# Optimization experiments

Hardware: AMD Instinct MI355X
Metric: run time of the kernel (lower is better)

## Reference

```python
import jax, jax.numpy as jnp
import numpy as np


def _pairwise_dist(x, y):
    # x: [B, N, D], y: [B, M, D] -> [B, N, M] Euclidean distances.
    # Use ||x||^2 + ||y||^2 - 2<x,y> (gram form) to avoid the [B,N,M,D]
    # broadcast intermediate the torch code materializes.
    x2 = jnp.sum(x * x, axis=-1)  # [B, N]
    y2 = jnp.sum(y * y, axis=-1)  # [B, M]
    xy = jnp.einsum('bnd,bmd->bnm', x, y)  # [B, N, M]
    sq = x2[:, :, None] + y2[:, None, :] - 2.0 * xy
    return jnp.sqrt(jnp.maximum(sq, 1e-12))


def setup_inputs() -> dict:
    key = jax.random.key(0)
    k1, k2 = jax.random.split(key)
    B, N, M, D = 8, 4096, 4096, 64
    pred = jax.random.normal(k1, (B, N, D), dtype=jnp.float32)
    label = jax.random.normal(k2, (B, M, D), dtype=jnp.float32)
    return {"pred": pred, "label": label}


def reference(pred, label):
    dis = _pairwise_dist(pred, label)  # [B, N, M]
    dis_xy = jnp.max(jnp.min(dis, axis=2))  # max over all (b, n) of min over m
    dis_yx = jnp.max(jnp.min(dis, axis=1))  # max over all (b, m) of min over n
    return dis_xy + dis_yx
```

## Files before the change

kernel.cpp:

```cpp
#include <hip/hip_runtime.h>
#include <hip/hip_bf16.h>

#define B_ 8
#define N_ 4096
#define M_ 4096
#define D_ 64
#define BNT (B_ * N_)
#define BMT (B_ * M_)
#define TA 64
#define TB 128
#define NT 512
#define CHUNK_TILES 8
#define CHUNK_B (TB * CHUNK_TILES)
#define MCHUNK (M_ / CHUNK_B)
#define NBLK (N_ / TA * MCHUNK * B_)

typedef short bf16x8 __attribute__((ext_vector_type(8)));
typedef float f32x4 __attribute__((ext_vector_type(4)));

__device__ __forceinline__ unsigned short f2bf(float f) {
  __hip_bfloat16 h = __float2bfloat16(f);
  return *reinterpret_cast<unsigned short*>(&h);
}

__device__ __forceinline__ unsigned fkey(float f) {
  unsigned b = __float_as_uint(f);
  return b ^ ((unsigned)((int)b >> 31) | 0x80000000u);
}
__device__ __forceinline__ float funkey(unsigned k) {
  unsigned b = (k & 0x80000000u) ? (k ^ 0x80000000u) : ~k;
  return __uint_as_float(b);
}

__device__ __forceinline__ bf16x8 cvt8(float4 lo, float4 hi) {
  union { unsigned short u[8]; bf16x8 v; } r;
  r.u[0] = f2bf(lo.x); r.u[1] = f2bf(lo.y); r.u[2] = f2bf(lo.z); r.u[3] = f2bf(lo.w);
  r.u[4] = f2bf(hi.x); r.u[5] = f2bf(hi.y); r.u[6] = f2bf(hi.z); r.u[7] = f2bf(hi.w);
  return r.v;
}

__device__ __forceinline__ void gload_lds16(const void* g, void* l) {
  __builtin_amdgcn_global_load_lds(
      (const __attribute__((address_space(1))) unsigned int*)g,
      (__attribute__((address_space(3))) unsigned int*)l, 16, 0, 0);
}

template <int ROWS, bool BF>
__device__ __forceinline__ void stage_tile(const void* gsrc, unsigned short* lds,
                                           int t, int srcpat) {
  if (BF) {
    constexpr int PER_WAVE = (ROWS * 128 / 1024) / (NT / 64);
    const char* gp = (const char*)gsrc;
    int w = t >> 6;
#pragma unroll
    for (int i = 0; i < PER_WAVE; i++) {
      int q = w * PER_WAVE + i;
      gload_lds16(gp + q * 1024 + srcpat, (char*)lds + q * 1024);
    }
  } else {
    const float4* g4 = (const float4*)gsrc;
#pragma unroll
    for (int i = 0; i < ROWS * 16 / NT; i++) {
      int off = i * NT + t;
      float4 v = g4[off];
      int row = off >> 4;
      int cb = (off & 15) * 8;
      int ba = (row * 128 + cb) ^ ((row & 7) << 4);
      ushort4 p;
      p.x = f2bf(v.x); p.y = f2bf(v.y); p.z = f2bf(v.z); p.w = f2bf(v.w);
      *(ushort4*)((char*)lds + ba) = p;
    }
  }
}

template <bool CONV>
__global__ __launch_bounds__(256) void prep_kernel(
    const float* __restrict__ pred, const float* __restrict__ label,
    unsigned short* __restrict__ predbf, unsigned short* __restrict__ labelbf,
    float* __restrict__ x2, float* __restrict__ y2,
    unsigned* __restrict__ minN, unsigned* __restrict__ minM,
    unsigned* __restrict__ gmax) {
  int t = threadIdx.x;
  int lane = t & 15;
  long row = (long)blockIdx.x * 16 + (t >> 4);
  bool isA = row < BNT;
  const float4* src;
  unsigned short* bdst;
  float* ndst;
  unsigned* mdst;
  if (isA) {
    src = (const float4*)(pred + row * D_);
    bdst = predbf + row * D_;
    ndst = x2 + row;
    mdst = minN + row;
  } else {
    long r2 = row - BNT;
    src = (const float4*)(label + r2 * D_);
    bdst = labelbf + r2 * D_;
    ndst = y2 + r2;
    mdst = minM + r2;
  }
  float4 v = src[lane];
  if (CONV) {
    float s = isA ? -2.f : 1.f;
    ushort4 p;
    p.x = f2bf(s * v.x); p.y = f2bf(s * v.y);
    p.z = f2bf(s * v.z); p.w = f2bf(s * v.w);
    *(ushort4*)(bdst + lane * 4) = p;
  }
  float s = v.x * v.x + v.y * v.y + v.z * v.z + v.w * v.w;
  s += __shfl_xor(s, 1);
  s += __shfl_xor(s, 2);
  s += __shfl_xor(s, 4);
  s += __shfl_xor(s, 8);
  if (lane == 0) {
    *ndst = s;
    *mdst = 0xFFFFFFFFu;
  }
  if (blockIdx.x == 0 && t < 2) gmax[t] = 0u;
}

template <bool BF>
__global__ __launch_bounds__(NT) void fused_kernel(
    const void* __restrict__ Asrc, const void* __restrict__ Bsrc,
    const float* __restrict__ x2g, const float* __restrict__ y2g,
    unsigned* __restrict__ minN, unsigned* __restrict__ minM) {
  __shared__ alignas(16) unsigned short Bs[2][TB * 64];
  __shared__ float y2l[CHUNK_B];
  __shared__ float cmSlab[CHUNK_B];
  __shared__ float red[8][TA];

  const int t = threadIdx.x;
  const int bid = blockIdx.x;
  const int k = bid & 7;
  const int j = bid >> 3;
  const int b = k;
  const int yq = j >> 6;
  const int x = j & 63;
  const int a0 = x * TA;
  const int m0 = yq * CHUNK_B;

  const int w = t >> 6, l = t & 63;
  const int g = l >> 4, c = l & 15;
  const int srcpat = (l >> 3) * 128 + (((l & 7) * 16) ^ ((l >> 3) << 4));

  const size_t rowbytes = BF ? 128 : 256;
  const char* Bgl = (const char*)Bsrc + ((size_t)b * M_ + m0) * rowbytes;

  ((float2*)y2l)[t] = ((const float2*)(y2g + (size_t)b * M_ + m0))[t];

  stage_tile<TB, BF>(Bgl, Bs[0], t, srcpat);

  bf16x8 af[2][4];
  if (BF) {
    const unsigned short* Ab =
        (const unsigned short*)Asrc + ((size_t)b * N_ + a0) * D_;
#pragma unroll
    for (int kk = 0; kk < 2; kk++)
#pragma unroll
      for (int mi = 0; mi < 4; mi++)
        af[kk][mi] =
            *(const bf16x8*)(Ab + (size_t)(mi * 16 + c) * D_ + kk * 32 + g * 8);
  } else {
    const float* Af = (const float*)Asrc + ((size_t)b * N_ + a0) * D_;
#pragma unroll
    for (int kk = 0; kk < 2; kk++)
#pragma unroll
      for (int mi = 0; mi < 4; mi++) {
        const float4* p =
            (const float4*)(Af + (size_t)(mi * 16 + c) * D_ + kk * 32 + g * 8);
        float4 lo = p[0], hi = p[1];
        lo.x *= -2.f; lo.y *= -2.f; lo.z *= -2.f; lo.w *= -2.f;
        hi.x *= -2.f; hi.y *= -2.f; hi.z *= -2.f; hi.w *= -2.f;
        af[kk][mi] = cvt8(lo, hi);
      }
  }

  float x2v[4][4];
#pragma unroll
  for (int mi = 0; mi < 4; mi++)
#pragma unroll
    for (int e = 0; e < 4; e++)
      x2v[mi][e] = x2g[(size_t)b * N_ + a0 + mi * 16 + g * 4 + e];

  float rmin[4][4];
#pragma unroll
  for (int mi = 0; mi < 4; mi++)
#pragma unroll
    for (int e = 0; e < 4; e++) rmin[mi][e] = INFINITY;

  __syncthreads();

  for (int it = 0; it < CHUNK_TILES; it++) {
    if (it + 1 < CHUNK_TILES)
      stage_tile<TB, BF>(Bgl + (size_t)(it + 1) * TB * rowbytes,
                         Bs[(it + 1) & 1], t, srcpat);
    const char* Bcur = (const char*)(&Bs[it & 1][0]);

    const int r = w * 16 + c;
    const float nv = y2l[it * TB + r];
    bf16x8 b0 = *(const bf16x8*)(Bcur + ((r * 128 + g * 16) ^ ((r & 7) << 4)));
    bf16x8 b1 = *(const bf16x8*)(Bcur + ((r * 128 + 64 + g * 16) ^ ((r & 7) << 4)));

    f32x4 acc[4];
#pragma unroll
    for (int mi = 0; mi < 4; mi++) acc[mi] = (f32x4){nv, nv, nv, nv};
#pragma unroll
    for (int mi = 0; mi < 4; mi++)
      acc[mi] = __builtin_amdgcn_mfma_f32_16x16x32_bf16(af[0][mi], b0, acc[mi], 0, 0, 0);
#pragma unroll
    for (int mi = 0; mi < 4; mi++)
      acc[mi] = __builtin_amdgcn_mfma_f32_16x16x32_bf16(af[1][mi], b1, acc[mi], 0, 0, 0);

    float cs[4];
#pragma unroll
    for (int mi = 0; mi < 4; mi++) {
      float c0 = acc[mi][0] + x2v[mi][0];
      float c1 = acc[mi][1] + x2v[mi][1];
      float c2 = acc[mi][2] + x2v[mi][2];
      float c3 = acc[mi][3] + x2v[mi][3];
      cs[mi] = fminf(fminf(c0, c1), fminf(c2, c3));
#pragma unroll
      for (int e = 0; e < 4; e++)
        rmin[mi][e] = fminf(rmin[mi][e], acc[mi][e]);
    }
    float cm = fminf(fminf(cs[0], cs[1]), fminf(cs[2], cs[3]));
    cm = fminf(cm, __shfl_xor(cm, 16));
    cm = fminf(cm, __shfl_xor(cm, 32));
    if (g == 0) cmSlab[it * TB + r] = cm - nv;

    __syncthreads();
  }

#pragma unroll
  for (int mi = 0; mi < 4; mi++)
#pragma unroll
    for (int e = 0; e < 4; e++) {
      float r = rmin[mi][e];
      r = fminf(r, __shfl_xor(r, 1));
      r = fminf(r, __shfl_xor(r, 2));
      r = fminf(r, __shfl_xor(r, 4));
      r = fminf(r, __shfl_xor(r, 8));
      rmin[mi][e] = r;
    }
  if (c == 0) {
#pragma unroll
    for (int mi = 0; mi < 4; mi++)
#pragma unroll
      for (int e = 0; e < 4; e++)
        red[w][mi * 16 + g * 4 + e] = rmin[mi][e];
  }
  __syncthreads();
  if (t < TA) {
    float m = red[0][t];
#pragma unroll
    for (int i = 1; i < 8; i++) m = fminf(m, red[i][t]);
    atomicMin(&minN[(size_t)b * N_ + a0 + t], fkey(m));
  }
#pragma unroll
  for (int i = 0; i < CHUNK_B / NT; i++) {
    int r = i * NT + t;
    atomicMin(&minM[(size_t)b * M_ + m0 + r], fkey(cmSlab[r]));
  }
}

__global__ __launch_bounds__(256) void final1_kernel(
    const unsigned* __restrict__ minN, const unsigned* __restrict__ minM,
    const float* __restrict__ x2, const float* __restrict__ y2,
    unsigned* __restrict__ gmax) {
  int dir = blockIdx.x >> 5;
  int blk = blockIdx.x & 31;
  const unsigned* src = dir ? minM : minN;
  const float* nrm = dir ? y2 : x2;
  size_t base = (size_t)blk * 256;
  float mx = -INFINITY;
  {
    int i = threadIdx.x;
    uint4 k = ((const uint4*)src)[base + i];
    float4 nv = ((const float4*)nrm)[base + i];
    mx = fmaxf(mx, nv.x + funkey(k.x));
    mx = fmaxf(mx, nv.y + funkey(k.y));
    mx = fmaxf(mx, nv.z + funkey(k.z));
    mx = fmaxf(mx, nv.w + funkey(k.w));
  }
#pragma unroll
  for (int mask = 1; mask < 64; mask <<= 1) mx = fmaxf(mx, __shfl_xor(mx, mask));
  __shared__ float sm[4];
  if ((threadIdx.x & 63) == 0) sm[threadIdx.x >> 6] = mx;
  __syncthreads();
  if (threadIdx.x == 0) {
    mx = fmaxf(fmaxf(sm[0], sm[1]), fmaxf(sm[2], sm[3]));
    atomicMax(&gmax[dir], fkey(mx));
  }
}

__global__ void final2_kernel(const unsigned* __restrict__ gmax, float* __restrict__ out) {
  if (threadIdx.x == 0)
    out[0] = sqrtf(fmaxf(funkey(gmax[0]), 1e-12f)) +
             sqrtf(fmaxf(funkey(gmax[1]), 1e-12f));
}

extern "C" void kernel_launch(void* const* d_in, const int* in_sizes, int n_in,
                              void* d_out, int out_size, void* d_ws, size_t ws_size,
                              hipStream_t stream) {
  const float* pred = (const float*)d_in[0];
  const float* label = (const float*)d_in[1];
  char* ws = (char*)d_ws;

  const size_t bfBytes = (size_t)BNT * D_ * 2;
  const size_t needFast = 2 * bfBytes + (size_t)(BNT + BMT) * 8 + 64;

  if (ws_size >= needFast) {
    unsigned short* predbf = (unsigned short*)ws;
    unsigned short* labelbf = (unsigned short*)(ws + bfBytes);
    float* x2 = (float*)(ws + 2 * bfBytes);
    float* y2 = x2 + BNT;
    unsigned* minN = (unsigned*)(y2 + BMT);
    unsigned* minM = minN + BNT;
    unsigned* gmax = minM + BMT;

    prep_kernel<true><<<(BNT + BMT) / 16, 256, 0, stream>>>(
        pred, label, predbf, labelbf, x2, y2, minN, minM, gmax);
    fused_kernel<true><<<NBLK, NT, 0, stream>>>(
        predbf, labelbf, x2, y2, minN, minM);
    final1_kernel<<<64, 256, 0, stream>>>(minN, minM, x2, y2, gmax);
    final2_kernel<<<1, 64, 0, stream>>>(gmax, (float*)d_out);
  } else {
    float* x2 = (float*)ws;
    float* y2 = x2 + BNT;
    unsigned* minN = (unsigned*)(y2 + BMT);
    unsigned* minM = minN + BNT;
    unsigned* gmax = minM + BMT;

    prep_kernel<false><<<(BNT + BMT) / 16, 256, 0, stream>>>(
        pred, label, nullptr, nullptr, x2, y2, minN, minM, gmax);
    fused_kernel<false><<<NBLK, NT, 0, stream>>>(
        pred, label, x2, y2, minN, minM);
    final1_kernel<<<64, 256, 0, stream>>>(minN, minM, x2, y2, gmax);
    final2_kernel<<<1, 64, 0, stream>>>(gmax, (float*)d_out);
  }
}
```

Baseline: 72.70 us.

## Halve block size and stage B tiles via registers with two-deep prefetch

Drops the block to 256 threads, so each wave now covers two 16-row slices of every B tile, which doubles the MFMA work per wave. Global-to-LDS direct loads are replaced by register staging: tiles are prefetched two iterations ahead into registers, then written swizzled into LDS behind a lighter barrier. The aim is to hide global latency and cut barrier overhead per unit of work. In exchange it uses more registers, which may lower occupancy, and adds extra LDS write instructions.

```diff
diff --git a/kernel.cpp b/kernel.cpp
--- a/kernel.cpp
+++ b/kernel.cpp
@@ -9,7 +9,7 @@
 #define BMT (B_ * M_)
 #define TA 64
 #define TB 128
-#define NT 512
+#define NT 256
 #define CHUNK_TILES 8
 #define CHUNK_B (TB * CHUNK_TILES)
 #define MCHUNK (M_ / CHUNK_B)
@@ -39,37 +39,33 @@
   return r.v;
 }
 
-__device__ __forceinline__ void gload_lds16(const void* g, void* l) {
-  __builtin_amdgcn_global_load_lds(
-      (const __attribute__((address_space(1))) unsigned int*)g,
-      (__attribute__((address_space(3))) unsigned int*)l, 16, 0, 0);
-}
-
-template <int ROWS, bool BF>
-__device__ __forceinline__ void stage_tile(const void* gsrc, unsigned short* lds,
-                                           int t, int srcpat) {
-  if (BF) {
-    constexpr int PER_WAVE = (ROWS * 128 / 1024) / (NT / 64);
-    const char* gp = (const char*)gsrc;
-    int w = t >> 6;
-#pragma unroll
-    for (int i = 0; i < PER_WAVE; i++) {
-      int q = w * PER_WAVE + i;
-      gload_lds16(gp + q * 1024 + srcpat, (char*)lds + q * 1024);
+__device__ __forceinline__ void block_sync_lds() {
+  asm volatile("s_waitcnt lgkmcnt(0)" ::: "memory");
+  __builtin_amdgcn_s_barrier();
+  __builtin_amdgcn_sched_barrier(0);
+}
+
+template <bool BF>
+__device__ __forceinline__ void stage_load(const char* gtile, bf16x8* arr, int t) {
+#pragma unroll
+  for (int i = 0; i < 4; i++) {
+    int q = i * NT + t;
+    if (BF) {
+      arr[i] = *(const bf16x8*)(gtile + (size_t)q * 16);
+    } else {
+      const float4* p = (const float4*)(gtile + (size_t)q * 32);
+      arr[i] = cvt8(p[0], p[1]);
     }
-  } else {
-    const float4* g4 = (const float4*)gsrc;
-#pragma unroll
-    for (int i = 0; i < ROWS * 16 / NT; i++) {
-      int off = i * NT + t;
-      float4 v = g4[off];
-      int row = off >> 4;
-      int cb = (off & 15) * 8;
-      int ba = (row * 128 + cb) ^ ((row & 7) << 4);
-      ushort4 p;
-      p.x = f2bf(v.x); p.y = f2bf(v.y); p.z = f2bf(v.z); p.w = f2bf(v.w);
-      *(ushort4*)((char*)lds + ba) = p;
-    }
+  }
+}
+
+__device__ __forceinline__ void stage_write(unsigned short* lds, const bf16x8* arr, int t) {
+#pragma unroll
+  for (int i = 0; i < 4; i++) {
+    int q = i * NT + t;
+    int row = q >> 3, col = q & 7;
+    int dst = (row * 128 + col * 16) ^ ((row & 7) << 4);
+    *(bf16x8*)((char*)lds + dst) = arr[i];
   }
 }
 
@@ -128,28 +124,26 @@
   __shared__ alignas(16) unsigned short Bs[2][TB * 64];
   __shared__ float y2l[CHUNK_B];
   __shared__ float cmSlab[CHUNK_B];
-  __shared__ float red[8][TA];
+  __shared__ float red[4][TA];
 
   const int t = threadIdx.x;
   const int bid = blockIdx.x;
-  const int k = bid & 7;
+  const int b = bid & 7;
   const int j = bid >> 3;
-  const int b = k;
-  const int yq = j >> 6;
-  const int x = j & 63;
-  const int a0 = x * TA;
-  const int m0 = yq * CHUNK_B;
+  const int a0 = (j & 63) * TA;
+  const int m0 = (j >> 6) * CHUNK_B;
 
   const int w = t >> 6, l = t & 63;
   const int g = l >> 4, c = l & 15;
-  const int srcpat = (l >> 3) * 128 + (((l & 7) * 16) ^ ((l >> 3) << 4));
-
-  const size_t rowbytes = BF ? 128 : 256;
-  const char* Bgl = (const char*)Bsrc + ((size_t)b * M_ + m0) * rowbytes;
-
-  ((float2*)y2l)[t] = ((const float2*)(y2g + (size_t)b * M_ + m0))[t];
-
-  stage_tile<TB, BF>(Bgl, Bs[0], t, srcpat);
+
+  const size_t tilebytes = (size_t)TB * 64 * (BF ? 2 : 4);
+  const char* Bgl = (const char*)Bsrc + ((size_t)b * M_ + m0) * (BF ? 128 : 256);
+
+  ((float4*)y2l)[t] = ((const float4*)(y2g + (size_t)b * M_ + m0))[t];
+
+  bf16x8 stg[2][4];
+  stage_load<BF>(Bgl, stg[0], t);
+  stage_load<BF>(Bgl + tilebytes, stg[1], t);
 
   bf16x8 af[2][4];
   if (BF) {
@@ -189,47 +183,54 @@
 #pragma unroll
     for (int e = 0; e < 4; e++) rmin[mi][e] = INFINITY;
 
-  __syncthreads();
-
-  for (int it = 0; it < CHUNK_TILES; it++) {
-    if (it + 1 < CHUNK_TILES)
-      stage_tile<TB, BF>(Bgl + (size_t)(it + 1) * TB * rowbytes,
-                         Bs[(it + 1) & 1], t, srcpat);
+  stage_write(Bs[0], stg[0], t);
+  block_sync_lds();
+
+#pragma unroll
+  for (int it = 0; it < CHUNK_TILES; ++it) {
+    if (it + 2 < CHUNK_TILES)
+      stage_load<BF>(Bgl + (size_t)(it + 2) * tilebytes, stg[it & 1], t);
+
     const char* Bcur = (const char*)(&Bs[it & 1][0]);
-
-    const int r = w * 16 + c;
-    const float nv = y2l[it * TB + r];
-    bf16x8 b0 = *(const bf16x8*)(Bcur + ((r * 128 + g * 16) ^ ((r & 7) << 4)));
-    bf16x8 b1 = *(const bf16x8*)(Bcur + ((r * 128 + 64 + g * 16) ^ ((r & 7) << 4)));
-
-    f32x4 acc[4];
-#pragma unroll
-    for (int mi = 0; mi < 4; mi++) acc[mi] = (f32x4){nv, nv, nv, nv};
-#pragma unroll
-    for (int mi = 0; mi < 4; mi++)
-      acc[mi] = __builtin_amdgcn_mfma_f32_16x16x32_bf16(af[0][mi], b0, acc[mi], 0, 0, 0);
-#pragma unroll
-    for (int mi = 0; mi < 4; mi++)
-      acc[mi] = __builtin_amdgcn_mfma_f32_16x16x32_bf16(af[1][mi], b1, acc[mi], 0, 0, 0);
-
-    float cs[4];
-#pragma unroll
-    for (int mi = 0; mi < 4; mi++) {
-      float c0 = acc[mi][0] + x2v[mi][0];
-      float c1 = acc[mi][1] + x2v[mi][1];
-      float c2 = acc[mi][2] + x2v[mi][2];
-      float c3 = acc[mi][3] + x2v[mi][3];
-      cs[mi] = fminf(fminf(c0, c1), fminf(c2, c3));
-#pragma unroll
-      for (int e = 0; e < 4; e++)
-        rmin[mi][e] = fminf(rmin[mi][e], acc[mi][e]);
+#pragma unroll
+    for (int h = 0; h < 2; ++h) {
+      const int r = w * 32 + h * 16 + c;
+      const float nv = y2l[it * TB + r];
+      bf16x8 b0 = *(const bf16x8*)(Bcur + ((r * 128 + g * 16) ^ ((r & 7) << 4)));
+      bf16x8 b1 = *(const bf16x8*)(Bcur + ((r * 128 + 64 + g * 16) ^ ((r & 7) << 4)));
+
+      f32x4 acc[4];
+#pragma unroll
+      for (int mi = 0; mi < 4; mi++) acc[mi] = (f32x4){nv, nv, nv, nv};
+#pragma unroll
+      for (int mi = 0; mi < 4; mi++)
+        acc[mi] = __builtin_amdgcn_mfma_f32_16x16x32_bf16(af[0][mi], b0, acc[mi], 0, 0, 0);
+#pragma unroll
+      for (int mi = 0; mi < 4; mi++)
+        acc[mi] = __builtin_amdgcn_mfma_f32_16x16x32_bf16(af[1][mi], b1, acc[mi], 0, 0, 0);
+
+      float cs[4];
+#pragma unroll
+      for (int mi = 0; mi < 4; mi++) {
+        float c0 = acc[mi][0] + x2v[mi][0];
+        float c1 = acc[mi][1] + x2v[mi][1];
+        float c2 = acc[mi][2] + x2v[mi][2];
+        float c3 = acc[mi][3] + x2v[mi][3];
+        cs[mi] = fminf(fminf(c0, c1), fminf(c2, c3));
+#pragma unroll
+        for (int e = 0; e < 4; e++)
+          rmin[mi][e] = fminf(rmin[mi][e], acc[mi][e]);
+      }
+      float cm = fminf(fminf(cs[0], cs[1]), fminf(cs[2], cs[3]));
+      cm = fminf(cm, __shfl_xor(cm, 16));
+      cm = fminf(cm, __shfl_xor(cm, 32));
+      if (g == 0) cmSlab[it * TB + r] = cm - nv;
     }
-    float cm = fminf(fminf(cs[0], cs[1]), fminf(cs[2], cs[3]));
-    cm = fminf(cm, __shfl_xor(cm, 16));
-    cm = fminf(cm, __shfl_xor(cm, 32));
-    if (g == 0) cmSlab[it * TB + r] = cm - nv;
-
-    __syncthreads();
+
+    if (it + 1 < CHUNK_TILES) {
+      stage_write(Bs[(it + 1) & 1], stg[(it + 1) & 1], t);
+      block_sync_lds();
+    }
   }
 
 #pragma unroll
@@ -252,9 +253,7 @@
   }
   __syncthreads();
   if (t < TA) {
-    float m = red[0][t];
-#pragma unroll
-    for (int i = 1; i < 8; i++) m = fminf(m, red[i][t]);
+    float m = fminf(fminf(red[0][t], red[1][t]), fminf(red[2][t], red[3][t]));
     atomicMin(&minN[(size_t)b * N_ + a0 + t], fkey(m));
   }
 #pragma unroll
```

New measurement: 87.50 us. 20.4% more time.
